# Kernel tuning notes

Hardware: AMD Instinct MI355X
Metric: run time of the kernel (lower is better)

## Reference

```python
import jax, jax.numpy as jnp
import numpy as np

B, F, T, DEPTH, C = 65536, 256, 256, 6, 4  # batch, n_features, num_trees, max_depth, n_classes


def setup_inputs() -> dict:
    key = jax.random.key(0)
    ks = jax.random.split(key, 4 + 2 * (DEPTH - 1))
    inp = {
        "x": jax.random.normal(ks[0], (B, F), dtype=jnp.float32),
        "root_nodes": jax.random.randint(ks[1], (T,), 0, F, dtype=jnp.int32),
        "root_biases": jax.random.normal(ks[2], (T,), dtype=jnp.float32),
        "leaf_nodes": jax.random.normal(ks[3], (T * 2 ** DEPTH, C), dtype=jnp.float32),
    }
    for lvl in range(1, DEPTH):
        n = T * 2 ** lvl  # flattened tree-major level table
        inp[f"nodes_{lvl}"] = jax.random.randint(ks[2 + 2 * lvl], (n,), 0, F, dtype=jnp.int32)
        inp[f"biases_{lvl}"] = jax.random.normal(ks[3 + 2 * lvl], (n,), dtype=jnp.float32)
    return inp


def _forward(x, root_nodes, root_biases, level_nodes, level_biases, leaf_nodes):
    Bx = x.shape[0]
    Tn = root_nodes.shape[0]
    tree_idx = jnp.arange(Tn, dtype=jnp.int32) * 2  # torch tree_indices
    # root split: [B, T] -> flat [B*T], value = tree*2 + bit
    prev = (jnp.take(x, root_nodes, axis=1) >= root_biases).astype(jnp.int32) + tree_idx
    prev = prev.reshape(-1)
    for nodes, biases in zip(level_nodes, level_biases):
        gidx = jnp.take(nodes, prev).reshape(Bx, Tn)          # feature index per (row, tree)
        feats = jnp.take_along_axis(x, gidx, axis=1).reshape(-1)
        prev = 2 * prev + (feats >= jnp.take(biases, prev)).astype(jnp.int32)
    out = jnp.take(leaf_nodes, prev, axis=0).reshape(Bx, Tn, -1)  # [B, T, C]
    return out


def reference(x, root_nodes, root_biases, leaf_nodes,
              nodes_1, biases_1, nodes_2, biases_2, nodes_3, biases_3,
              nodes_4, biases_4, nodes_5, biases_5):
    out = _forward(
        x, root_nodes, root_biases,
        (nodes_1, nodes_2, nodes_3, nodes_4, nodes_5),
        (biases_1, biases_2, biases_3, biases_4, biases_5),
        leaf_nodes,
    )
    # classification path: aggregation/calibration are identity, classes are 0..C-1
    # so perform_class_select is False -> return (argmax over dim=1, output)
    return (jnp.argmax(out, axis=1), out)
```

## Files before the change

kernel.cpp:

```cpp
#include <hip/hip_runtime.h>
#include <hip/hip_bf16.h>

#define NB 65536
#define NF 256
#define NT 256
#define NC 4
#define NG 8
#define TG 32
#define RB 128
#define RPB (NB / RB)
#define RPC 16
#define NCHUNK (RPB / RPC)
#define NTHREADS 256

__device__ __forceinline__ unsigned int mono32(float v) {
    unsigned int u = __float_as_uint(v);
    return (u & 0x80000000u) ? ~u : (u | 0x80000000u);
}

__global__ __launch_bounds__(NTHREADS, 4) void k_traverse(
    const float* __restrict__ x,
    const int*   __restrict__ root_nodes, const float* __restrict__ root_biases,
    const float* __restrict__ leaf_nodes,
    const int* __restrict__ n1, const float* __restrict__ b1,
    const int* __restrict__ n2, const float* __restrict__ b2,
    const int* __restrict__ n3, const float* __restrict__ b3,
    const int* __restrict__ n4, const float* __restrict__ b4,
    const int* __restrict__ n5, const float* __restrict__ b5,
    float* __restrict__ out_val,
    unsigned long long* __restrict__ keys)
{
    const int g  = blockIdx.x >> 7;
    const int rb = blockIdx.x & (RB - 1);

    __shared__ int2  tbl[1792];
    __shared__ float xr[RPC * NF];

    const int tid = threadIdx.x;
    const int rs  = tid >> 5;
    const int lt  = tid & 31;
    const int t   = g * TG + lt;

    const int2 e0   = make_int2(root_nodes[t], __float_as_int(root_biases[t]));
    const int2 e1_0 = make_int2(n1[2 * t],     __float_as_int(b1[2 * t]));
    const int2 e1_1 = make_int2(n1[2 * t + 1], __float_as_int(b1[2 * t + 1]));
    const int2 e2_0 = make_int2(n2[4 * t],     __float_as_int(b2[4 * t]));
    const int2 e2_1 = make_int2(n2[4 * t + 1], __float_as_int(b2[4 * t + 1]));
    const int2 e2_2 = make_int2(n2[4 * t + 2], __float_as_int(b2[4 * t + 2]));
    const int2 e2_3 = make_int2(n2[4 * t + 3], __float_as_int(b2[4 * t + 3]));

    tbl[tid] = make_int2(n3[g * 256 + tid], __float_as_int(b3[g * 256 + tid]));
    #pragma unroll
    for (int k = 0; k < 2; ++k) {
        const int i = tid + 256 * k;
        tbl[256 + i] = make_int2(n4[g * 512 + i], __float_as_int(b4[g * 512 + i]));
    }
    #pragma unroll
    for (int k = 0; k < 4; ++k) {
        const int i = tid + 256 * k;
        tbl[768 + i] = make_int2(n5[g * 1024 + i], __float_as_int(b5[g * 1024 + i]));
    }

    const float4* xg  = (const float4*)x;
    const float4* lf4 = (const float4*)leaf_nodes;
    float4*       ov4 = (float4*)out_val;
    const int halfshift = tid & 32;

    for (int ck = 0; ck < NCHUNK; ++ck) {
        const int r0 = rb * RPB + ck * RPC;

        {
            const size_t base4 = (size_t)r0 * (NF / 4);
            float4* xr4 = (float4*)xr;
            #pragma unroll
            for (int k = 0; k < 4; ++k)
                xr4[tid + 256 * k] = xg[base4 + tid + 256 * k];
        }
        __syncthreads();

        const float* xrow0 = xr + rs * NF;
        const float* xrow1 = xr + (rs + 8) * NF;
        int p0, p1;
        int2 ea, eb;

        p0 = (xrow0[e0.x] >= __int_as_float(e0.y)) ? 1 : 0;
        p1 = (xrow1[e0.x] >= __int_as_float(e0.y)) ? 1 : 0;
        ea = p0 ? e1_1 : e1_0;
        eb = p1 ? e1_1 : e1_0;
        p0 = 2 * p0 + (xrow0[ea.x] >= __int_as_float(ea.y) ? 1 : 0);
        p1 = 2 * p1 + (xrow1[eb.x] >= __int_as_float(eb.y) ? 1 : 0);
        {
            int2 a0 = (p0 & 1) ? e2_1 : e2_0, a1 = (p0 & 1) ? e2_3 : e2_2;
            ea = (p0 & 2) ? a1 : a0;
            int2 c0 = (p1 & 1) ? e2_1 : e2_0, c1 = (p1 & 1) ? e2_3 : e2_2;
            eb = (p1 & 2) ? c1 : c0;
        }
        p0 = 2 * p0 + (xrow0[ea.x] >= __int_as_float(ea.y) ? 1 : 0);
        p1 = 2 * p1 + (xrow1[eb.x] >= __int_as_float(eb.y) ? 1 : 0);
        ea = tbl[(lt << 3) + p0];
        eb = tbl[(lt << 3) + p1];
        p0 = 2 * p0 + (xrow0[ea.x] >= __int_as_float(ea.y) ? 1 : 0);
        p1 = 2 * p1 + (xrow1[eb.x] >= __int_as_float(eb.y) ? 1 : 0);
        ea = tbl[256 + (lt << 4) + p0];
        eb = tbl[256 + (lt << 4) + p1];
        p0 = 2 * p0 + (xrow0[ea.x] >= __int_as_float(ea.y) ? 1 : 0);
        p1 = 2 * p1 + (xrow1[eb.x] >= __int_as_float(eb.y) ? 1 : 0);
        ea = tbl[768 + (lt << 5) + p0];
        eb = tbl[768 + (lt << 5) + p1];
        p0 = 2 * p0 + (xrow0[ea.x] >= __int_as_float(ea.y) ? 1 : 0);
        p1 = 2 * p1 + (xrow1[eb.x] >= __int_as_float(eb.y) ? 1 : 0);

        const float4 leaf0 = lf4[(size_t)g * 2048 + (lt << 6) + p0];
        const float4 leaf1 = lf4[(size_t)g * 2048 + (lt << 6) + p1];
        ov4[(size_t)(r0 + rs)     * NT + t] = leaf0;
        ov4[(size_t)(r0 + rs + 8) * NT + t] = leaf1;

        #pragma unroll
        for (int c = 0; c < 2; ++c) {
            const float4 lv = c ? leaf1 : leaf0;
            const int row = r0 + rs + 8 * c;
            unsigned long long kk[4];
            const float vc[4] = { lv.x, lv.y, lv.z, lv.w };
            #pragma unroll
            for (int cls = 0; cls < 4; ++cls) {
                float m = vc[cls];
                #pragma unroll
                for (int msk = 16; msk >= 1; msk >>= 1)
                    m = fmaxf(m, __shfl_xor(m, msk));
                const unsigned long long ball = __ballot(vc[cls] == m);
                const unsigned int hm = (unsigned int)(ball >> halfshift);
                const int gidx = g * TG + (__ffs(hm) - 1);
                kk[cls] = ((unsigned long long)mono32(m) << 8) |
                          (unsigned long long)(255 - gidx);
            }
            if (lt < 4) {
                unsigned long long k = (lt == 0) ? kk[0] :
                                       (lt == 1) ? kk[1] :
                                       (lt == 2) ? kk[2] : kk[3];
                atomicMax(&keys[(size_t)row * NC + lt], k);
            }
        }
        __syncthreads();
    }
}

__global__ __launch_bounds__(256) void k_finish(
    const unsigned long long* __restrict__ keys,
    float* __restrict__ out_arg)
{
    const int i = blockIdx.x * 256 + threadIdx.x;
    out_arg[i] = (float)(255 - (int)(keys[i] & 0xFFull));
}

extern "C" void kernel_launch(void* const* d_in, const int* in_sizes, int n_in,
                              void* d_out, int out_size, void* d_ws, size_t ws_size,
                              hipStream_t stream) {
    const float* x           = (const float*)d_in[0];
    const int*   root_nodes  = (const int*)  d_in[1];
    const float* root_biases = (const float*)d_in[2];
    const float* leaf_nodes  = (const float*)d_in[3];
    const int*   n1 = (const int*)  d_in[4];
    const float* b1 = (const float*)d_in[5];
    const int*   n2 = (const int*)  d_in[6];
    const float* b2 = (const float*)d_in[7];
    const int*   n3 = (const int*)  d_in[8];
    const float* b3 = (const float*)d_in[9];
    const int*   n4 = (const int*)  d_in[10];
    const float* b4 = (const float*)d_in[11];
    const int*   n5 = (const int*)  d_in[12];
    const float* b5 = (const float*)d_in[13];

    float* out_arg = (float*)d_out;
    float* out_val = (float*)d_out + (size_t)NB * NC;
    unsigned long long* keys = (unsigned long long*)d_ws;

    hipMemsetAsync(d_ws, 0, (size_t)NB * NC * sizeof(unsigned long long), stream);

    k_traverse<<<NG * RB, NTHREADS, 0, stream>>>(
        x, root_nodes, root_biases, leaf_nodes,
        n1, b1, n2, b2, n3, b3, n4, b4, n5, b5,
        out_val, keys);

    k_finish<<<(NB * NC) / 256, 256, 0, stream>>>(keys, out_arg);
}
```

Before: 417.2 us.

## Transpose LDS node tables, use direct global-to-LDS loads, merge class max reductions

Stores the level-3/4/5 node tables in shared memory transposed, node-major with the tree index innermost, so lanes of different trees read consecutive addresses and LDS bank conflicts drop. The x row chunk is now copied with global_load_lds straight into shared memory, skipping the round trip through registers. The four per-class warp max reductions are packed into one butterfly that splits classes across lane groups, cutting the shuffle count. The direct LDS load relies on hardware-specific builtin semantics and on the existing syncthreads for ordering.

New measurement: 415.2 us. No clear change (-0.5%).

```diff
diff --git a/kernel.cpp b/kernel.cpp
--- a/kernel.cpp
+++ b/kernel.cpp
@@ -49,16 +49,22 @@
     const int2 e2_2 = make_int2(n2[4 * t + 2], __float_as_int(b2[4 * t + 2]));
     const int2 e2_3 = make_int2(n2[4 * t + 3], __float_as_int(b2[4 * t + 3]));
 
-    tbl[tid] = make_int2(n3[g * 256 + tid], __float_as_int(b3[g * 256 + tid]));
+    {
+        const int i = tid;
+        tbl[((i & 7) << 5) | (i >> 3)] =
+            make_int2(n3[g * 256 + i], __float_as_int(b3[g * 256 + i]));
+    }
     #pragma unroll
     for (int k = 0; k < 2; ++k) {
         const int i = tid + 256 * k;
-        tbl[256 + i] = make_int2(n4[g * 512 + i], __float_as_int(b4[g * 512 + i]));
+        tbl[256 + ((i & 15) << 5) + (i >> 4)] =
+            make_int2(n4[g * 512 + i], __float_as_int(b4[g * 512 + i]));
     }
     #pragma unroll
     for (int k = 0; k < 4; ++k) {
         const int i = tid + 256 * k;
-        tbl[768 + i] = make_int2(n5[g * 1024 + i], __float_as_int(b5[g * 1024 + i]));
+        tbl[768 + ((i & 31) << 5) + (i >> 5)] =
+            make_int2(n5[g * 1024 + i], __float_as_int(b5[g * 1024 + i]));
     }
 
     const float4* xg  = (const float4*)x;
@@ -73,8 +79,12 @@
             const size_t base4 = (size_t)r0 * (NF / 4);
             float4* xr4 = (float4*)xr;
             #pragma unroll
-            for (int k = 0; k < 4; ++k)
-                xr4[tid + 256 * k] = xg[base4 + tid + 256 * k];
+            for (int k = 0; k < 4; ++k) {
+                __builtin_amdgcn_global_load_lds(
+                    (const __attribute__((address_space(1))) void*)(xg + base4 + tid + 256 * k),
+                    (__attribute__((address_space(3))) void*)(xr4 + tid + 256 * k),
+                    16, 0, 0);
+            }
         }
         __syncthreads();
 
@@ -97,16 +107,16 @@
         }
         p0 = 2 * p0 + (xrow0[ea.x] >= __int_as_float(ea.y) ? 1 : 0);
         p1 = 2 * p1 + (xrow1[eb.x] >= __int_as_float(eb.y) ? 1 : 0);
-        ea = tbl[(lt << 3) + p0];
-        eb = tbl[(lt << 3) + p1];
-        p0 = 2 * p0 + (xrow0[ea.x] >= __int_as_float(ea.y) ? 1 : 0);
-        p1 = 2 * p1 + (xrow1[eb.x] >= __int_as_float(eb.y) ? 1 : 0);
-        ea = tbl[256 + (lt << 4) + p0];
-        eb = tbl[256 + (lt << 4) + p1];
-        p0 = 2 * p0 + (xrow0[ea.x] >= __int_as_float(ea.y) ? 1 : 0);
-        p1 = 2 * p1 + (xrow1[eb.x] >= __int_as_float(eb.y) ? 1 : 0);
-        ea = tbl[768 + (lt << 5) + p0];
-        eb = tbl[768 + (lt << 5) + p1];
+        ea = tbl[(p0 << 5) + lt];
+        eb = tbl[(p1 << 5) + lt];
+        p0 = 2 * p0 + (xrow0[ea.x] >= __int_as_float(ea.y) ? 1 : 0);
+        p1 = 2 * p1 + (xrow1[eb.x] >= __int_as_float(eb.y) ? 1 : 0);
+        ea = tbl[256 + (p0 << 5) + lt];
+        eb = tbl[256 + (p1 << 5) + lt];
+        p0 = 2 * p0 + (xrow0[ea.x] >= __int_as_float(ea.y) ? 1 : 0);
+        p1 = 2 * p1 + (xrow1[eb.x] >= __int_as_float(eb.y) ? 1 : 0);
+        ea = tbl[768 + (p0 << 5) + lt];
+        eb = tbl[768 + (p1 << 5) + lt];
         p0 = 2 * p0 + (xrow0[ea.x] >= __int_as_float(ea.y) ? 1 : 0);
         p1 = 2 * p1 + (xrow1[eb.x] >= __int_as_float(eb.y) ? 1 : 0);
 
@@ -116,35 +126,45 @@
         ov4[(size_t)(r0 + rs + 8) * NT + t] = leaf1;
 
         #pragma unroll
-        for (int c = 0; c < 2; ++c) {
-            const float4 lv = c ? leaf1 : leaf0;
-            const int row = r0 + rs + 8 * c;
-            unsigned long long kk[4];
-            const float vc[4] = { lv.x, lv.y, lv.z, lv.w };
+        for (int c2 = 0; c2 < 2; ++c2) {
+            const float4 lv = c2 ? leaf1 : leaf0;
+            const int row = r0 + rs + 8 * c2;
+            const float vc0 = lv.x, vc1 = lv.y, vc2 = lv.z, vc3 = lv.w;
+
+            const float a0 = fmaxf(vc0, __shfl_xor(vc0, 16));
+            const float a1 = fmaxf(vc1, __shfl_xor(vc1, 16));
+            const float a2 = fmaxf(vc2, __shfl_xor(vc2, 16));
+            const float a3 = fmaxf(vc3, __shfl_xor(vc3, 16));
+            const bool hi4 = (lt & 16) != 0;
+            float u = hi4 ? a2 : a0;
+            float w = hi4 ? a3 : a1;
+            const float mu = fmaxf(u, __shfl_xor(u, 8));
+            const float mw = fmaxf(w, __shfl_xor(w, 8));
+            float v = (lt & 8) ? mw : mu;
+            v = fmaxf(v, __shfl_xor(v, 4));
+            v = fmaxf(v, __shfl_xor(v, 2));
+            v = fmaxf(v, __shfl_xor(v, 1));
+
+            const float vcarr[4] = { vc0, vc1, vc2, vc3 };
+            unsigned long long kk = 0;
             #pragma unroll
             for (int cls = 0; cls < 4; ++cls) {
-                float m = vc[cls];
-                #pragma unroll
-                for (int msk = 16; msk >= 1; msk >>= 1)
-                    m = fmaxf(m, __shfl_xor(m, msk));
-                const unsigned long long ball = __ballot(vc[cls] == m);
+                const float mc = __shfl(v, halfshift + (cls << 3));
+                const unsigned long long ball = __ballot(vcarr[cls] == mc);
                 const unsigned int hm = (unsigned int)(ball >> halfshift);
                 const int gidx = g * TG + (__ffs(hm) - 1);
-                kk[cls] = ((unsigned long long)mono32(m) << 8) |
-                          (unsigned long long)(255 - gidx);
+                const unsigned long long kc =
+                    ((unsigned long long)mono32(mc) << 8) |
+                    (unsigned long long)(255 - gidx);
+                if (lt == cls) kk = kc;
             }
-            if (lt < 4) {
-                unsigned long long k = (lt == 0) ? kk[0] :
-                                       (lt == 1) ? kk[1] :
-                                       (lt == 2) ? kk[2] : kk[3];
-                atomicMax(&keys[(size_t)row * NC + lt], k);
-            }
+            if (lt < 4) atomicMax(&keys[(size_t)row * NC + lt], kk);
         }
         __syncthreads();
     }
 }
 
-__global__ __launch_bounds__(256) void k_finish(
+__global__ void __launch_bounds__(256) k_finish(
     const unsigned long long* __restrict__ keys,
     float* __restrict__ out_arg)
 {
```
